# Optimization experiments

Hardware: AMD Instinct MI355X
Metric: run time of the kernel (lower is better)

## Reference

```python
import jax, jax.numpy as jnp
import numpy as np

B, S, D, H = 4, 4096, 512, 64

def setup_inputs() -> dict:
    key = jax.random.key(0)
    ks = jax.random.split(key, 7)
    x = jax.random.normal(ks[0], (B, S, D), dtype=jnp.float32)
    Wq = jax.random.normal(ks[1], (D, H), dtype=jnp.float32) / np.sqrt(D)
    bq = jax.random.normal(ks[2], (H,), dtype=jnp.float32) * 0.01
    Wk = jax.random.normal(ks[3], (D, H), dtype=jnp.float32) / np.sqrt(D)
    bk = jax.random.normal(ks[4], (H,), dtype=jnp.float32) * 0.01
    Wv = jax.random.normal(ks[5], (D, H), dtype=jnp.float32) / np.sqrt(D)
    bv = jax.random.normal(ks[6], (H,), dtype=jnp.float32) * 0.01
    return {"x": x, "Wq": Wq, "bq": bq, "Wk": Wk, "bk": bk, "Wv": Wv, "bv": bv}

def reference(x, Wq, bq, Wk, bk, Wv, bv):
    # q,k,v: [B,S,H]
    q = jnp.einsum('bsd,dh->bsh', x, Wq) + bq
    k = jnp.einsum('bsd,dh->bsh', x, Wk) + bk
    v = jnp.einsum('bsd,dh->bsh', x, Wv) + bv
    H_dim = q.shape[-1]
    scores = jnp.einsum('bqh,bkh->bqk', q, k) / jnp.sqrt(jnp.float32(H_dim))  # [B,S,S]
    attn = jax.nn.softmax(scores, axis=-1)
    return jnp.einsum('bqk,bkh->bqh', attn, v)  # [B,S,H]
```

## Files before the change

### kernel.cpp

```cpp
#include <hip/hip_runtime.h>
#include <math.h>

using short8  = __attribute__((ext_vector_type(8))) short;
using floatx4 = __attribute__((ext_vector_type(4))) float;

#define B_DIM 4
#define S_DIM 4096
#define D_DIM 512
#define H_DIM 64
#define NROWS (B_DIM * S_DIM)

#define QSCALE 0.18033688011112042f
#define FMAX   16.0f

__device__ __forceinline__ unsigned short f2bf(float f) {
  unsigned int u = __builtin_bit_cast(unsigned int, f);
  u += 0x7fffu + ((u >> 16) & 1u);
  return (unsigned short)(u >> 16);
}

__device__ __forceinline__ unsigned int pack_bf2(float lo, float hi) {
#if __has_builtin(__builtin_amdgcn_perm)
  return __builtin_amdgcn_perm(__builtin_bit_cast(unsigned int, hi),
                               __builtin_bit_cast(unsigned int, lo), 0x07060302u);
#else
  return (__builtin_bit_cast(unsigned int, hi) & 0xFFFF0000u) |
         (__builtin_bit_cast(unsigned int, lo) >> 16);
#endif
}

#if __has_builtin(__builtin_amdgcn_exp2f)
#define EXP2(x) __builtin_amdgcn_exp2f(x)
#else
#define EXP2(x) exp2f(x)
#endif

__global__ __launch_bounds__(256) void wprep(
    const float* __restrict__ Wq, const float* __restrict__ Wk,
    const float* __restrict__ Wv, unsigned short* __restrict__ Wf)
{
  const int t = blockIdx.x * 256 + threadIdx.x;
  if (t >= 3 * 16 * 4 * 64) return;
  const int lane = t & 63;
  const int f    = t >> 6;
  const int nt   = f & 3;
  const int ks   = (f >> 2) & 15;
  const int pi   = f >> 6;
  const int qq   = lane >> 4;
  const int cc   = lane & 15;
  const float* W = (pi == 0) ? Wq : (pi == 1) ? Wk : Wv;
  const float* src = W + (ks * 32 + qq * 8) * H_DIM + (nt * 16 + cc);
  short8 v;
#pragma unroll
  for (int j = 0; j < 8; ++j) v[j] = (short)f2bf(src[j * H_DIM]);
  *(short8*)(Wf + t * 8) = v;
}

__global__ __launch_bounds__(128) void qkv_proj(
    const float* __restrict__ x, const unsigned short* __restrict__ Wf,
    const float* __restrict__ bq, const float* __restrict__ bk,
    const float* __restrict__ bv,
    unsigned short* __restrict__ Qf, unsigned short* __restrict__ Kf,
    unsigned short* __restrict__ Vf)
{
  __shared__ alignas(16) unsigned short QL[32 * 72];
  __shared__ alignas(16) unsigned short KL[32 * 72];
  __shared__ alignas(16) unsigned short VTL[64 * 40];

  const int tid  = threadIdx.x;
  const int lane = tid & 63;
  const int w    = tid >> 6;
  const int qq   = lane >> 4;
  const int cc   = lane & 15;
  const int rowblk = blockIdx.x * 32;

  floatx4 acc[3][4] = {};
  const int arow = rowblk + w * 16 + cc;
  const float* xrow = x + arow * D_DIM;

  short8 wb[2][12];
  float4 xb[2][2];

  {
#pragma unroll
    for (int pi = 0; pi < 3; ++pi)
#pragma unroll
      for (int nt = 0; nt < 4; ++nt)
        wb[0][pi * 4 + nt] = *(const short8*)(Wf + (((pi * 16 + 0) * 4 + nt) * 64 + lane) * 8);
    const float4* xp = (const float4*)(xrow + qq * 8);
    xb[0][0] = xp[0]; xb[0][1] = xp[1];
  }

#pragma unroll
  for (int ks = 0; ks < 16; ++ks) {
    const int cur = ks & 1;
    if (ks < 15) {
#pragma unroll
      for (int pi = 0; pi < 3; ++pi)
#pragma unroll
        for (int nt = 0; nt < 4; ++nt)
          wb[cur ^ 1][pi * 4 + nt] = *(const short8*)(Wf + (((pi * 16 + ks + 1) * 4 + nt) * 64 + lane) * 8);
      const float4* xp = (const float4*)(xrow + (ks + 1) * 32 + qq * 8);
      xb[cur ^ 1][0] = xp[0]; xb[cur ^ 1][1] = xp[1];
    }
    short8 af;
    {
      float4 x0 = xb[cur][0], x1 = xb[cur][1];
      af[0] = (short)f2bf(x0.x); af[1] = (short)f2bf(x0.y);
      af[2] = (short)f2bf(x0.z); af[3] = (short)f2bf(x0.w);
      af[4] = (short)f2bf(x1.x); af[5] = (short)f2bf(x1.y);
      af[6] = (short)f2bf(x1.z); af[7] = (short)f2bf(x1.w);
    }
#pragma unroll
    for (int pi = 0; pi < 3; ++pi)
#pragma unroll
      for (int nt = 0; nt < 4; ++nt)
        acc[pi][nt] = __builtin_amdgcn_mfma_f32_16x16x32_bf16(af, wb[cur][pi * 4 + nt], acc[pi][nt], 0, 0, 0);
  }

#pragma unroll
  for (int nt = 0; nt < 4; ++nt) {
    const int h = nt * 16 + cc;
    const float vbq = bq[h], vbk = bk[h], vbv = bv[h];
#pragma unroll
    for (int r = 0; r < 4; ++r) {
      const int row = w * 16 + qq * 4 + r;
      QL[row * 72 + h] = f2bf((acc[0][nt][r] + vbq) * QSCALE);
      KL[row * 72 + h] = f2bf(acc[1][nt][r] + vbk);
      VTL[h * 40 + row] = f2bf(acc[2][nt][r] + vbv);
    }
  }
  __syncthreads();

#pragma unroll
  for (int rep = 0; rep < 2; ++rep) {
    const int c   = rep * 128 + tid;
    const int qtl = c >> 7;
    const int hf  = (c >> 6) & 1;
    const int lc  = c & 63;
    const int qqc = lc >> 4, ccc = lc & 15;
    const int gt  = (rowblk >> 4) + qtl;
    short8 vq = *(const short8*)&QL[(qtl * 16 + ccc) * 72 + hf * 32 + qqc * 8];
    *(short8*)(Qf + ((gt * 2 + hf) * 64 + lc) * 8) = vq;
    short8 vk = *(const short8*)&KL[(qtl * 16 + ccc) * 72 + hf * 32 + qqc * 8];
    *(short8*)(Kf + ((gt * 2 + hf) * 64 + lc) * 8) = vk;
  }
#pragma unroll
  for (int rep = 0; rep < 2; ++rep) {
    const int c   = rep * 128 + tid;
    const int nt  = c >> 6;
    const int qqv = (c >> 4) & 3;
    const int ccv = c & 15;
    const int gc  = rowblk >> 6;
    const int hf  = (rowblk >> 5) & 1;
    short8 vv;
#pragma unroll
    for (int j = 0; j < 8; ++j)
      vv[j] = (short)VTL[(nt * 16 + ccv) * 40 + qqv * 4 + (j >> 1) + ((j & 1) << 4)];
    *(short8*)(Vf + (((gc * 8) + nt * 2 + hf) * 64 + qqv * 16 + ccv) * 8) = vv;
  }
}

__global__ __launch_bounds__(512, 2) void flash_attn(
    const unsigned short* __restrict__ Qf, const unsigned short* __restrict__ Kf,
    const unsigned short* __restrict__ Vf, float* __restrict__ out)
{
  __shared__ alignas(16) unsigned int Pl[8][64 * 20];
  __shared__ float OB[4][64 * 65];
  __shared__ float LB[4][64];

  const int tid  = threadIdx.x;
  const int lane = tid & 63;
  const int w    = tid >> 6;
  const int qq   = lane >> 4;
  const int cc   = lane & 15;
  const int g    = blockIdx.x;
  const int b    = (g & 7) >> 1;
  const int qt64 = ((g >> 3) << 1) | (g & 1);
  const int qrow0 = qt64 * 64;
  const int gtq  = b * 256 + qt64 * 4;

  short8 aq[4][2];
#pragma unroll
  for (int qs = 0; qs < 4; ++qs)
#pragma unroll
    for (int hf = 0; hf < 2; ++hf)
      aq[qs][hf] = *(const short8*)(Qf + (((gtq + qs) * 2 + hf) * 64 + lane) * 8);

  short8 vone;
#pragma unroll
  for (int j = 0; j < 8; ++j) vone[j] = (short)0x3F80;

  floatx4 O[4][4] = {};
  floatx4 O5[4] = {};
  unsigned int* Pw = &Pl[w][0];
  const unsigned short* Pr = (const unsigned short*)Pw;
  const floatx4 zero = {};
  const int kstart = w * 512;

  short8 bkb[2][2][2], bvb[2][4];
  {
    const int kb = kstart;
    const int kt = b * 256 + (kb >> 4);
    const int vp = (b * 64 + (kb >> 6)) * 8 + ((kb >> 5) & 1);
#pragma unroll
    for (int t = 0; t < 2; ++t)
#pragma unroll
      for (int hf = 0; hf < 2; ++hf)
        bkb[0][t][hf] = *(const short8*)(Kf + (((kt + t) * 2 + hf) * 64 + lane) * 8);
#pragma unroll
    for (int nt = 0; nt < 4; ++nt)
      bvb[0][nt] = *(const short8*)(Vf + ((vp + nt * 2) * 64 + lane) * 8);
  }

#pragma unroll 2
  for (int s = 0; s < 16; ++s) {
    const int cur = s & 1, nxt = cur ^ 1;
    if (s < 15) {
      const int kb = kstart + (s + 1) * 32;
      const int kt = b * 256 + (kb >> 4);
      const int vp = (b * 64 + (kb >> 6)) * 8 + ((kb >> 5) & 1);
#pragma unroll
      for (int t = 0; t < 2; ++t)
#pragma unroll
        for (int hf = 0; hf < 2; ++hf)
          bkb[nxt][t][hf] = *(const short8*)(Kf + (((kt + t) * 2 + hf) * 64 + lane) * 8);
#pragma unroll
      for (int nt = 0; nt < 4; ++nt)
        bvb[nxt][nt] = *(const short8*)(Vf + ((vp + nt * 2) * 64 + lane) * 8);
    }
#pragma unroll
    for (int qs = 0; qs < 4; ++qs) {
      floatx4 s0 = __builtin_amdgcn_mfma_f32_16x16x32_bf16(aq[qs][0], bkb[cur][0][0], zero, 0, 0, 0);
      s0 = __builtin_amdgcn_mfma_f32_16x16x32_bf16(aq[qs][1], bkb[cur][0][1], s0, 0, 0, 0);
      floatx4 s1 = __builtin_amdgcn_mfma_f32_16x16x32_bf16(aq[qs][0], bkb[cur][1][0], zero, 0, 0, 0);
      s1 = __builtin_amdgcn_mfma_f32_16x16x32_bf16(aq[qs][1], bkb[cur][1][1], s1, 0, 0, 0);
#pragma unroll
      for (int r = 0; r < 4; ++r) {
        float p0 = EXP2(s0[r] - FMAX);
        float p1 = EXP2(s1[r] - FMAX);
        Pw[(qs * 16 + qq * 4 + r) * 20 + cc] = pack_bf2(p0, p1);
      }
    }
#pragma unroll
    for (int qs = 0; qs < 4; ++qs) {
      const short8 ap = *(const short8*)(Pr + (qs * 16 + cc) * 40 + qq * 8);
#pragma unroll
      for (int nt = 0; nt < 4; ++nt)
        O[qs][nt] = __builtin_amdgcn_mfma_f32_16x16x32_bf16(ap, bvb[cur][nt], O[qs][nt], 0, 0, 0);
      O5[qs] = __builtin_amdgcn_mfma_f32_16x16x32_bf16(ap, vone, O5[qs], 0, 0, 0);
    }
  }

  float lr[4][4];
#pragma unroll
  for (int qs = 0; qs < 4; ++qs)
#pragma unroll
    for (int r = 0; r < 4; ++r) lr[qs][r] = O5[qs][r];

  if (w >= 4) {
    float* Ob = OB[w - 4];
#pragma unroll
    for (int qs = 0; qs < 4; ++qs)
#pragma unroll
      for (int nt = 0; nt < 4; ++nt)
#pragma unroll
        for (int r = 0; r < 4; ++r)
          Ob[(qs * 16 + qq * 4 + r) * 65 + nt * 16 + cc] = O[qs][nt][r];
    if (cc == 0)
#pragma unroll
      for (int qs = 0; qs < 4; ++qs)
#pragma unroll
        for (int r = 0; r < 4; ++r) LB[w - 4][qs * 16 + qq * 4 + r] = lr[qs][r];
  }
  __syncthreads();
  if (w < 4) {
    const float* Ob = OB[w];
#pragma unroll
    for (int qs = 0; qs < 4; ++qs)
#pragma unroll
      for (int nt = 0; nt < 4; ++nt)
#pragma unroll
        for (int r = 0; r < 4; ++r)
          O[qs][nt][r] += Ob[(qs * 16 + qq * 4 + r) * 65 + nt * 16 + cc];
#pragma unroll
    for (int qs = 0; qs < 4; ++qs)
#pragma unroll
      for (int r = 0; r < 4; ++r) lr[qs][r] += LB[w][qs * 16 + qq * 4 + r];
  }
  __syncthreads();
  if (w == 2 || w == 3) {
    float* Ob = OB[w - 2];
#pragma unroll
    for (int qs = 0; qs < 4; ++qs)
#pragma unroll
      for (int nt = 0; nt < 4; ++nt)
#pragma unroll
        for (int r = 0; r < 4; ++r)
          Ob[(qs * 16 + qq * 4 + r) * 65 + nt * 16 + cc] = O[qs][nt][r];
    if (cc == 0)
#pragma unroll
      for (int qs = 0; qs < 4; ++qs)
#pragma unroll
        for (int r = 0; r < 4; ++r) LB[w - 2][qs * 16 + qq * 4 + r] = lr[qs][r];
  }
  __syncthreads();
  if (w < 2) {
    const float* Ob = OB[w];
#pragma unroll
    for (int qs = 0; qs < 4; ++qs)
#pragma unroll
      for (int nt = 0; nt < 4; ++nt)
#pragma unroll
        for (int r = 0; r < 4; ++r)
          O[qs][nt][r] += Ob[(qs * 16 + qq * 4 + r) * 65 + nt * 16 + cc];
#pragma unroll
    for (int qs = 0; qs < 4; ++qs)
#pragma unroll
      for (int r = 0; r < 4; ++r) lr[qs][r] += LB[w][qs * 16 + qq * 4 + r];
  }
  __syncthreads();
  if (w == 1) {
    float* Ob = OB[0];
#pragma unroll
    for (int qs = 0; qs < 4; ++qs)
#pragma unroll
      for (int nt = 0; nt < 4; ++nt)
#pragma unroll
        for (int r = 0; r < 4; ++r)
          Ob[(qs * 16 + qq * 4 + r) * 65 + nt * 16 + cc] = O[qs][nt][r];
    if (cc == 0)
#pragma unroll
      for (int qs = 0; qs < 4; ++qs)
#pragma unroll
        for (int r = 0; r < 4; ++r) LB[0][qs * 16 + qq * 4 + r] = lr[qs][r];
  }
  __syncthreads();
  if (w == 0) {
    const float* Ob = OB[0];
#pragma unroll
    for (int qs = 0; qs < 4; ++qs) {
#pragma unroll
      for (int r = 0; r < 4; ++r) {
        const float lt  = lr[qs][r] + LB[0][qs * 16 + qq * 4 + r];
        const float inv = 1.0f / lt;
        const int rowg  = b * S_DIM + qrow0 + qs * 16 + qq * 4 + r;
#pragma unroll
        for (int nt = 0; nt < 4; ++nt) {
          const float o = O[qs][nt][r] + Ob[(qs * 16 + qq * 4 + r) * 65 + nt * 16 + cc];
          out[rowg * H_DIM + nt * 16 + cc] = o * inv;
        }
      }
    }
  }
}

extern "C" void kernel_launch(void* const* d_in, const int* in_sizes, int n_in,
                              void* d_out, int out_size, void* d_ws, size_t ws_size,
                              hipStream_t stream) {
  const float* x  = (const float*)d_in[0];
  const float* Wq = (const float*)d_in[1];
  const float* bq = (const float*)d_in[2];
  const float* Wk = (const float*)d_in[3];
  const float* bk = (const float*)d_in[4];
  const float* Wv = (const float*)d_in[5];
  const float* bv = (const float*)d_in[6];
  float* out = (float*)d_out;

  unsigned short* Qf = (unsigned short*)d_ws;
  unsigned short* Kf = Qf + NROWS * H_DIM;
  unsigned short* Vf = Kf + NROWS * H_DIM;
  unsigned short* Wf = Vf + NROWS * H_DIM;

  wprep<<<48, 256, 0, stream>>>(Wq, Wk, Wv, Wf);
  qkv_proj<<<512, 128, 0, stream>>>(x, Wf, bq, bk, bv, Qf, Kf, Vf);
  flash_attn<<<256, 512, 0, stream>>>(Qf, Kf, Vf, out);
}
```

Baseline: 117.4 us.

## Software-pipeline QK^T/exp with PV via double-buffered P tiles, drop ones-MFMA row sum

Restructures the per-wave loop so scores and exponentials for the next key block are computed after issuing the PV MFMAs for the current block, using a double-buffered per-wave LDS P tile. Row sums are now accumulated in fp32 registers and reduced with cross-lane shuffles instead of an extra MFMA against a ones vector. P reads become 128-bit uint loads. The loop is fully unrolled and the min-blocks launch bound is removed. This trades more registers and LDS for overlap of the exp work with the matrix unit, and may lower occupancy.

```diff
diff --git a/kernel.cpp b/kernel.cpp
--- a/kernel.cpp
+++ b/kernel.cpp
@@ -3,6 +3,7 @@
 
 using short8  = __attribute__((ext_vector_type(8))) short;
 using floatx4 = __attribute__((ext_vector_type(4))) float;
+using uintx4  = __attribute__((ext_vector_type(4))) unsigned int;
 
 #define B_DIM 4
 #define S_DIM 4096
@@ -161,11 +162,11 @@
   }
 }
 
-__global__ __launch_bounds__(512, 2) void flash_attn(
+__global__ __launch_bounds__(512) void flash_attn(
     const unsigned short* __restrict__ Qf, const unsigned short* __restrict__ Kf,
     const unsigned short* __restrict__ Vf, float* __restrict__ out)
 {
-  __shared__ alignas(16) unsigned int Pl[8][64 * 20];
+  __shared__ alignas(16) unsigned int Pl[8][2][64 * 20];
   __shared__ float OB[4][64 * 65];
   __shared__ float LB[4][64];
 
@@ -187,18 +188,14 @@
     for (int hf = 0; hf < 2; ++hf)
       aq[qs][hf] = *(const short8*)(Qf + (((gtq + qs) * 2 + hf) * 64 + lane) * 8);
 
-  short8 vone;
-#pragma unroll
-  for (int j = 0; j < 8; ++j) vone[j] = (short)0x3F80;
-
   floatx4 O[4][4] = {};
-  floatx4 O5[4] = {};
-  unsigned int* Pw = &Pl[w][0];
-  const unsigned short* Pr = (const unsigned short*)Pw;
+  float lr[4][4] = {};
   const floatx4 zero = {};
   const int kstart = w * 512;
 
-  short8 bkb[2][2][2], bvb[2][4];
+  short8 kf[2][2];
+  short8 vb[2][4];
+
   {
     const int kb = kstart;
     const int kt = b * 256 + (kb >> 4);
@@ -207,13 +204,28 @@
     for (int t = 0; t < 2; ++t)
 #pragma unroll
       for (int hf = 0; hf < 2; ++hf)
-        bkb[0][t][hf] = *(const short8*)(Kf + (((kt + t) * 2 + hf) * 64 + lane) * 8);
+        kf[t][hf] = *(const short8*)(Kf + (((kt + t) * 2 + hf) * 64 + lane) * 8);
 #pragma unroll
     for (int nt = 0; nt < 4; ++nt)
-      bvb[0][nt] = *(const short8*)(Vf + ((vp + nt * 2) * 64 + lane) * 8);
-  }
-
-#pragma unroll 2
+      vb[0][nt] = *(const short8*)(Vf + ((vp + nt * 2) * 64 + lane) * 8);
+    unsigned int* PwW = &Pl[w][0][0];
+#pragma unroll
+    for (int qs = 0; qs < 4; ++qs) {
+      floatx4 s0 = __builtin_amdgcn_mfma_f32_16x16x32_bf16(aq[qs][0], kf[0][0], zero, 0, 0, 0);
+      s0 = __builtin_amdgcn_mfma_f32_16x16x32_bf16(aq[qs][1], kf[0][1], s0, 0, 0, 0);
+      floatx4 s1 = __builtin_amdgcn_mfma_f32_16x16x32_bf16(aq[qs][0], kf[1][0], zero, 0, 0, 0);
+      s1 = __builtin_amdgcn_mfma_f32_16x16x32_bf16(aq[qs][1], kf[1][1], s1, 0, 0, 0);
+#pragma unroll
+      for (int r = 0; r < 4; ++r) {
+        float p0 = EXP2(s0[r] - FMAX);
+        float p1 = EXP2(s1[r] - FMAX);
+        lr[qs][r] += p0 + p1;
+        PwW[(qs * 16 + qq * 4 + r) * 20 + cc] = pack_bf2(p0, p1);
+      }
+    }
+  }
+
+#pragma unroll
   for (int s = 0; s < 16; ++s) {
     const int cur = s & 1, nxt = cur ^ 1;
     if (s < 15) {
@@ -224,39 +236,51 @@
       for (int t = 0; t < 2; ++t)
 #pragma unroll
         for (int hf = 0; hf < 2; ++hf)
-          bkb[nxt][t][hf] = *(const short8*)(Kf + (((kt + t) * 2 + hf) * 64 + lane) * 8);
-#pragma unroll
-      for (int nt = 0; nt < 4; ++nt)
-        bvb[nxt][nt] = *(const short8*)(Vf + ((vp + nt * 2) * 64 + lane) * 8);
-    }
+          kf[t][hf] = *(const short8*)(Kf + (((kt + t) * 2 + hf) * 64 + lane) * 8);
+#pragma unroll
+      for (int nt = 0; nt < 4; ++nt)
+        vb[nxt][nt] = *(const short8*)(Vf + ((vp + nt * 2) * 64 + lane) * 8);
+    }
+    const unsigned int* PwR = &Pl[w][cur][0];
+    short8 ap[4];
 #pragma unroll
     for (int qs = 0; qs < 4; ++qs) {
-      floatx4 s0 = __builtin_amdgcn_mfma_f32_16x16x32_bf16(aq[qs][0], bkb[cur][0][0], zero, 0, 0, 0);
-      s0 = __builtin_amdgcn_mfma_f32_16x16x32_bf16(aq[qs][1], bkb[cur][0][1], s0, 0, 0, 0);
-      floatx4 s1 = __builtin_amdgcn_mfma_f32_16x16x32_bf16(aq[qs][0], bkb[cur][1][0], zero, 0, 0, 0);
-      s1 = __builtin_amdgcn_mfma_f32_16x16x32_bf16(aq[qs][1], bkb[cur][1][1], s1, 0, 0, 0);
-#pragma unroll
-      for (int r = 0; r < 4; ++r) {
-        float p0 = EXP2(s0[r] - FMAX);
-        float p1 = EXP2(s1[r] - FMAX);
-        Pw[(qs * 16 + qq * 4 + r) * 20 + cc] = pack_bf2(p0, p1);
+      uintx4 t = *(const uintx4*)(PwR + (qs * 16 + cc) * 20 + qq * 4);
+      ap[qs] = __builtin_bit_cast(short8, t);
+    }
+#pragma unroll
+    for (int qs = 0; qs < 4; ++qs)
+#pragma unroll
+      for (int nt = 0; nt < 4; ++nt)
+        O[qs][nt] = __builtin_amdgcn_mfma_f32_16x16x32_bf16(ap[qs], vb[cur][nt], O[qs][nt], 0, 0, 0);
+    if (s < 15) {
+      unsigned int* PwW = &Pl[w][nxt][0];
+#pragma unroll
+      for (int qs = 0; qs < 4; ++qs) {
+        floatx4 s0 = __builtin_amdgcn_mfma_f32_16x16x32_bf16(aq[qs][0], kf[0][0], zero, 0, 0, 0);
+        s0 = __builtin_amdgcn_mfma_f32_16x16x32_bf16(aq[qs][1], kf[0][1], s0, 0, 0, 0);
+        floatx4 s1 = __builtin_amdgcn_mfma_f32_16x16x32_bf16(aq[qs][0], kf[1][0], zero, 0, 0, 0);
+        s1 = __builtin_amdgcn_mfma_f32_16x16x32_bf16(aq[qs][1], kf[1][1], s1, 0, 0, 0);
+#pragma unroll
+        for (int r = 0; r < 4; ++r) {
+          float p0 = EXP2(s0[r] - FMAX);
+          float p1 = EXP2(s1[r] - FMAX);
+          lr[qs][r] += p0 + p1;
+          PwW[(qs * 16 + qq * 4 + r) * 20 + cc] = pack_bf2(p0, p1);
+        }
       }
     }
-#pragma unroll
-    for (int qs = 0; qs < 4; ++qs) {
-      const short8 ap = *(const short8*)(Pr + (qs * 16 + cc) * 40 + qq * 8);
-#pragma unroll
-      for (int nt = 0; nt < 4; ++nt)
-        O[qs][nt] = __builtin_amdgcn_mfma_f32_16x16x32_bf16(ap, bvb[cur][nt], O[qs][nt], 0, 0, 0);
-      O5[qs] = __builtin_amdgcn_mfma_f32_16x16x32_bf16(ap, vone, O5[qs], 0, 0, 0);
-    }
-  }
-
-  float lr[4][4];
+  }
+
 #pragma unroll
   for (int qs = 0; qs < 4; ++qs)
 #pragma unroll
-    for (int r = 0; r < 4; ++r) lr[qs][r] = O5[qs][r];
+    for (int r = 0; r < 4; ++r) {
+      float v = lr[qs][r];
+      v += __shfl_xor(v, 1); v += __shfl_xor(v, 2);
+      v += __shfl_xor(v, 4); v += __shfl_xor(v, 8);
+      lr[qs][r] = v;
+    }
 
   if (w >= 4) {
     float* Ob = OB[w - 4];
```

New measurement: 130.2 us. +10.9%, slower.
